# Optimization experiments

Hardware: AMD Instinct MI355X
Metric: run time of the kernel (lower is better)

Reference implementation:

```python
import jax, jax.numpy as jnp
import numpy as np

EPS = 1e-9
THRESHOLD = 0.5


def _spatial_entropy(feat, w1, b1, w2, b2):
    # feat: [B, C, H, W]
    p = jax.nn.sigmoid(feat)
    # faithful to source: log(p+eps) - (1-p)*log(1-p+eps)
    ent = jnp.log(p + EPS) - (1.0 - p) * jnp.log(1.0 - p + EPS)  # [B,C,H,W]
    pooled = feat.mean(axis=(2, 3))                               # [B,C]
    h = jax.nn.relu(pooled @ w1 + b1)                             # [B,64]
    cw = jax.nn.sigmoid(h @ w2 + b2)                              # [B,C]
    se = jnp.einsum('bchw,bc->bhw', ent, cw)                      # [B,H,W]
    # F.normalize(x, dim=(1,2)): L2-normalize jointly over H,W
    norm = jnp.sqrt(jnp.sum(se * se, axis=(1, 2), keepdims=True))
    return se / jnp.maximum(norm, 1e-12)


def _low_entropy_mask(entropy_map):
    # entropy_map: [B,H,W] -> mask [B,1,H,W]
    thr = entropy_map.mean(axis=(1, 2), keepdims=True) * THRESHOLD
    return (entropy_map < thr).astype(entropy_map.dtype)[:, None, :, :]


def setup_inputs() -> dict:
    key = jax.random.key(0)
    k1, k2, k3, k4 = jax.random.split(key, 4)
    B, C, H, W = 16, 256, 64, 64
    vis_feat = jax.random.normal(k1, (B, C, H, W), dtype=jnp.float32)
    text_feat = jax.random.normal(k2, (B, C, H, W), dtype=jnp.float32)
    # channel attention MLP params (Linear(256,64) -> Linear(64,256))
    w1 = jax.random.normal(k3, (256, 64), dtype=jnp.float32) * 0.0625
    b1 = jnp.zeros((64,), dtype=jnp.float32)
    w2 = jax.random.normal(k4, (64, 256), dtype=jnp.float32) * 0.125
    b2 = jnp.zeros((256,), dtype=jnp.float32)
    return {"vis_feat": vis_feat, "text_feat": text_feat,
            "w1": w1, "b1": b1, "w2": w2, "b2": b2}


def reference(vis_feat, text_feat, w1, b1, w2, b2):
    vis_entropy = _spatial_entropy(vis_feat, w1, b1, w2, b2)    # [B,H,W]
    text_entropy = _spatial_entropy(text_feat, w1, b1, w2, b2)  # [B,H,W]
    vis_low = _low_entropy_mask(vis_entropy)                     # [B,1,H,W]
    text_low = _low_entropy_mask(text_entropy)                   # [B,1,H,W]
    enhanced = vis_feat * vis_low + text_feat * text_low * (1.0 - vis_low)
    return enhanced, vis_entropy, text_entropy
```

## Files before the change

kernel.cpp:

```cpp
#include <hip/hip_runtime.h>
#include <math.h>

#define B 16
#define C 256
#define HW 4096
#define EPSE 1e-9f
#define NTHREADS 256
#define CCHUNK 32

__device__ __forceinline__ float fast_rcp(float x) { return __builtin_amdgcn_rcpf(x); }

__device__ __forceinline__ float entf(float x) {
    float e  = __expf(-x);
    float p  = fast_rcp(1.f + e);
    float l1 = __logf(p + EPSE);
    float q  = 1.f - p;
    float l2 = __logf(q + EPSE);
    return fmaf(-q, l2, l1);
}

__global__ void k_pooled(const float* __restrict__ vis,
                         const float* __restrict__ txt,
                         float* __restrict__ pooled,
                         float* __restrict__ se) {
    int blk = blockIdx.x;
    if (blk < 128) {
        float4 z = make_float4(0.f, 0.f, 0.f, 0.f);
        ((float4*)se)[blk * NTHREADS + threadIdx.x] = z;
    }
    int f   = blk >> 12;
    int bc  = blk & (B * C - 1);
    const float* src = (f == 0 ? vis : txt) + (size_t)bc * HW;
    const float4* s4 = (const float4*)src;

    float s = 0.f;
    #pragma unroll
    for (int i = threadIdx.x; i < HW / 4; i += NTHREADS) {
        float4 v = s4[i];
        s += v.x + v.y + v.z + v.w;
    }
    for (int off = 32; off > 0; off >>= 1) s += __shfl_down(s, off);
    __shared__ float sm[4];
    if ((threadIdx.x & 63) == 0) sm[threadIdx.x >> 6] = s;
    __syncthreads();
    if (threadIdx.x == 0) {
        float tot = sm[0] + sm[1] + sm[2] + sm[3];
        pooled[blk] = tot * (1.0f / HW);
    }
}

__global__ void k_mlp(const float* __restrict__ pooled,
                      const float* __restrict__ w1, const float* __restrict__ b1,
                      const float* __restrict__ w2, const float* __restrict__ b2,
                      float* __restrict__ cw) {
    __shared__ float pl[B * C];
    __shared__ float h[B * 64];
    int f = blockIdx.x;
    const float* P = pooled + f * B * C;
    for (int i = threadIdx.x; i < B * C; i += NTHREADS) pl[i] = P[i];
    __syncthreads();
    for (int o = threadIdx.x; o < B * 64; o += NTHREADS) {
        int b = o >> 6, j = o & 63;
        float acc = b1[j];
        for (int c = 0; c < C; ++c) acc = fmaf(pl[b * C + c], w1[c * 64 + j], acc);
        h[o] = fmaxf(acc, 0.f);
    }
    __syncthreads();
    for (int o = threadIdx.x; o < B * C; o += NTHREADS) {
        int b = o >> 8, c2 = o & 255;
        float acc = b2[c2];
        for (int j = 0; j < 64; ++j) acc = fmaf(h[b * 64 + j], w2[j * 256 + c2], acc);
        cw[f * B * C + o] = fast_rcp(1.f + __expf(-acc));
    }
}

__global__ void k_se(const float* __restrict__ vis,
                     const float* __restrict__ txt,
                     const float* __restrict__ cw,
                     float* __restrict__ se) {
    int bx   = blockIdx.x;
    int cc   = bx & 7;
    int tile = (bx >> 3) & 3;
    int b    = (bx >> 5) & 15;
    int f    = bx >> 9;
    const float* src = (f == 0 ? vis : txt)
                       + (size_t)b * C * HW + (size_t)cc * CCHUNK * HW
                       + tile * 1024 + threadIdx.x * 4;

    __shared__ float cwl[CCHUNK];
    if (threadIdx.x < CCHUNK)
        cwl[threadIdx.x] = cw[f * B * C + b * C + cc * CCHUNK + threadIdx.x];
    __syncthreads();

    float4 acc = make_float4(0.f, 0.f, 0.f, 0.f);
    #pragma unroll 4
    for (int c = 0; c < CCHUNK; ++c) {
        float4 x = *(const float4*)(src + (size_t)c * HW);
        float w = cwl[c];
        acc.x = fmaf(entf(x.x), w, acc.x);
        acc.y = fmaf(entf(x.y), w, acc.y);
        acc.z = fmaf(entf(x.z), w, acc.z);
        acc.w = fmaf(entf(x.w), w, acc.w);
    }
    float* dst = se + (f * B + b) * HW + tile * 1024 + threadIdx.x * 4;
    atomicAdd(dst + 0, acc.x);
    atomicAdd(dst + 1, acc.y);
    atomicAdd(dst + 2, acc.z);
    atomicAdd(dst + 3, acc.w);
}

__global__ void k_stats(const float* __restrict__ se,
                        float* __restrict__ inv_norm,
                        float* __restrict__ thr) {
    int fb = blockIdx.x;
    const float4* s4 = (const float4*)(se + fb * HW);
    float s = 0.f, ss = 0.f;
    #pragma unroll
    for (int i = threadIdx.x; i < HW / 4; i += NTHREADS) {
        float4 v = s4[i];
        s  += v.x + v.y + v.z + v.w;
        ss = fmaf(v.x, v.x, ss); ss = fmaf(v.y, v.y, ss);
        ss = fmaf(v.z, v.z, ss); ss = fmaf(v.w, v.w, ss);
    }
    for (int off = 32; off > 0; off >>= 1) {
        s  += __shfl_down(s, off);
        ss += __shfl_down(ss, off);
    }
    __shared__ float sm[8];
    if ((threadIdx.x & 63) == 0) {
        sm[(threadIdx.x >> 6) * 2]     = s;
        sm[(threadIdx.x >> 6) * 2 + 1] = ss;
    }
    __syncthreads();
    if (threadIdx.x == 0) {
        float st  = sm[0] + sm[2] + sm[4] + sm[6];
        float sst = sm[1] + sm[3] + sm[5] + sm[7];
        inv_norm[fb] = 1.f / fmaxf(sqrtf(sst), 1e-12f);
        thr[fb]      = 0.5f * (st * (1.0f / HW));
    }
}

__global__ void k_selwrite(const float* __restrict__ se,
                           const float* __restrict__ inv_norm,
                           const float* __restrict__ thr,
                           float* __restrict__ out_ent_vis,
                           float* __restrict__ out_ent_text,
                           unsigned char* __restrict__ sel) {
    int id = blockIdx.x * NTHREADS + threadIdx.x;
    int b  = id >> 12;
    float sv = se[id];
    float st = se[B * HW + id];
    out_ent_vis[id]  = sv * inv_norm[b];
    out_ent_text[id] = st * inv_norm[B + b];
    bool vl = sv < thr[b];
    bool tl = st < thr[B + b];
    sel[id] = vl ? (unsigned char)1 : (tl ? (unsigned char)2 : (unsigned char)0);
}

__global__ void k_final(const float* __restrict__ vis,
                        const float* __restrict__ txt,
                        const unsigned char* __restrict__ sel,
                        float* __restrict__ out) {
    const int total4 = B * C * HW / 4;
    int stride = gridDim.x * blockDim.x;
    for (int i = blockIdx.x * blockDim.x + threadIdx.x; i < total4; i += stride) {
        float4 v = ((const float4*)vis)[i];
        float4 t = ((const float4*)txt)[i];
        int idx = i << 2;
        int b   = idx >> 20;
        int hw  = idx & (HW - 1);
        uchar4 s = *(const uchar4*)(sel + (b << 12) + hw);
        float4 o;
        o.x = (s.x == 1) ? v.x : ((s.x == 2) ? t.x : 0.f);
        o.y = (s.y == 1) ? v.y : ((s.y == 2) ? t.y : 0.f);
        o.z = (s.z == 1) ? v.z : ((s.z == 2) ? t.z : 0.f);
        o.w = (s.w == 1) ? v.w : ((s.w == 2) ? t.w : 0.f);
        ((float4*)out)[i] = o;
    }
}

extern "C" void kernel_launch(void* const* d_in, const int* in_sizes, int n_in,
                              void* d_out, int out_size, void* d_ws, size_t ws_size,
                              hipStream_t stream) {
    const float* vis = (const float*)d_in[0];
    const float* txt = (const float*)d_in[1];
    const float* w1  = (const float*)d_in[2];
    const float* b1  = (const float*)d_in[3];
    const float* w2  = (const float*)d_in[4];
    const float* b2  = (const float*)d_in[5];

    float* out_enh      = (float*)d_out;
    float* out_ent_vis  = out_enh + (size_t)B * C * HW;
    float* out_ent_text = out_ent_vis + B * HW;

    float* ws       = (float*)d_ws;
    float* pooled   = ws;
    float* cw       = ws + 8192;
    float* se       = ws + 16384;
    float* inv_norm = ws + 147456;
    float* thr      = ws + 147488;
    unsigned char* sel = (unsigned char*)(ws + 147520);

    k_pooled  <<<2 * B * C, NTHREADS, 0, stream>>>(vis, txt, pooled, se);
    k_mlp     <<<2,         NTHREADS, 0, stream>>>(pooled, w1, b1, w2, b2, cw);
    k_se      <<<1024,      NTHREADS, 0, stream>>>(vis, txt, cw, se);
    k_stats   <<<2 * B,     NTHREADS, 0, stream>>>(se, inv_norm, thr);
    k_selwrite<<<B * HW / NTHREADS, NTHREADS, 0, stream>>>(se, inv_norm, thr,
                                                           out_ent_vis, out_ent_text, sel);
    k_final   <<<2048,      NTHREADS, 0, stream>>>(vis, txt, sel, out_enh);
}
```

Before: 267.5 us.

## Fuse selection into final pass, per-wave pooling, smaller channel chunks, nontemporal stores

Removes the separate selection kernel and its byte mask: the final kernel now reads the entropy maps, computes the masks and normalized entropy outputs itself, and applies them over 16-channel groups with nontemporal stores. The pooling kernel assigns one wave per channel plane with four independent accumulators and no shared-memory reduction. The entropy kernel halves the channel chunk, doubling its grid to add parallelism at the cost of twice as many atomics. The intent is fewer launches, less intermediate traffic, and keeping the large output stream from polluting cache.

```diff
diff --git a/kernel.cpp b/kernel.cpp
--- a/kernel.cpp
+++ b/kernel.cpp
@@ -6,7 +6,14 @@
 #define HW 4096
 #define EPSE 1e-9f
 #define NTHREADS 256
-#define CCHUNK 32
+#define CCHUNK 16
+
+typedef float nfloat4 __attribute__((ext_vector_type(4)));
+
+__device__ __forceinline__ void nt_store4(float* p, float4 v) {
+    nfloat4 nv = { v.x, v.y, v.z, v.w };
+    __builtin_nontemporal_store(nv, (nfloat4*)p);
+}
 
 __device__ __forceinline__ float fast_rcp(float x) { return __builtin_amdgcn_rcpf(x); }
 
@@ -25,28 +32,29 @@
                          float* __restrict__ se) {
     int blk = blockIdx.x;
     if (blk < 128) {
-        float4 z = make_float4(0.f, 0.f, 0.f, 0.f);
-        ((float4*)se)[blk * NTHREADS + threadIdx.x] = z;
-    }
-    int f   = blk >> 12;
-    int bc  = blk & (B * C - 1);
-    const float* src = (f == 0 ? vis : txt) + (size_t)bc * HW;
-    const float4* s4 = (const float4*)src;
-
-    float s = 0.f;
+        ((float4*)se)[blk * NTHREADS + threadIdx.x] = make_float4(0.f, 0.f, 0.f, 0.f);
+    }
+    int wave = (blk << 2) | (threadIdx.x >> 6);
+    int lane = threadIdx.x & 63;
+    int f    = wave >> 12;
+    int bc   = wave & (B * C - 1);
+    const float4* src = (const float4*)((f == 0 ? vis : txt) + (size_t)bc * HW);
+
+    float s0 = 0.f, s1 = 0.f, s2 = 0.f, s3 = 0.f;
     #pragma unroll
-    for (int i = threadIdx.x; i < HW / 4; i += NTHREADS) {
-        float4 v = s4[i];
-        s += v.x + v.y + v.z + v.w;
-    }
+    for (int k = 0; k < 16; k += 4) {
+        float4 a = src[lane + (k + 0) * 64];
+        float4 b = src[lane + (k + 1) * 64];
+        float4 c = src[lane + (k + 2) * 64];
+        float4 d = src[lane + (k + 3) * 64];
+        s0 += a.x + a.y + a.z + a.w;
+        s1 += b.x + b.y + b.z + b.w;
+        s2 += c.x + c.y + c.z + c.w;
+        s3 += d.x + d.y + d.z + d.w;
+    }
+    float s = (s0 + s1) + (s2 + s3);
     for (int off = 32; off > 0; off >>= 1) s += __shfl_down(s, off);
-    __shared__ float sm[4];
-    if ((threadIdx.x & 63) == 0) sm[threadIdx.x >> 6] = s;
-    __syncthreads();
-    if (threadIdx.x == 0) {
-        float tot = sm[0] + sm[1] + sm[2] + sm[3];
-        pooled[blk] = tot * (1.0f / HW);
-    }
+    if (lane == 0) pooled[wave] = s * (1.0f / HW);
 }
 
 __global__ void k_mlp(const float* __restrict__ pooled,
@@ -79,10 +87,10 @@
                      const float* __restrict__ cw,
                      float* __restrict__ se) {
     int bx   = blockIdx.x;
-    int cc   = bx & 7;
-    int tile = (bx >> 3) & 3;
-    int b    = (bx >> 5) & 15;
-    int f    = bx >> 9;
+    int cc   = bx & 15;
+    int tile = (bx >> 4) & 3;
+    int b    = (bx >> 6) & 15;
+    int f    = bx >> 10;
     const float* src = (f == 0 ? vis : txt)
                        + (size_t)b * C * HW + (size_t)cc * CCHUNK * HW
                        + tile * 1024 + threadIdx.x * 4;
@@ -140,42 +148,51 @@
     }
 }
 
-__global__ void k_selwrite(const float* __restrict__ se,
-                           const float* __restrict__ inv_norm,
-                           const float* __restrict__ thr,
-                           float* __restrict__ out_ent_vis,
-                           float* __restrict__ out_ent_text,
-                           unsigned char* __restrict__ sel) {
-    int id = blockIdx.x * NTHREADS + threadIdx.x;
-    int b  = id >> 12;
-    float sv = se[id];
-    float st = se[B * HW + id];
-    out_ent_vis[id]  = sv * inv_norm[b];
-    out_ent_text[id] = st * inv_norm[B + b];
-    bool vl = sv < thr[b];
-    bool tl = st < thr[B + b];
-    sel[id] = vl ? (unsigned char)1 : (tl ? (unsigned char)2 : (unsigned char)0);
-}
-
 __global__ void k_final(const float* __restrict__ vis,
                         const float* __restrict__ txt,
-                        const unsigned char* __restrict__ sel,
-                        float* __restrict__ out) {
-    const int total4 = B * C * HW / 4;
-    int stride = gridDim.x * blockDim.x;
-    for (int i = blockIdx.x * blockDim.x + threadIdx.x; i < total4; i += stride) {
-        float4 v = ((const float4*)vis)[i];
-        float4 t = ((const float4*)txt)[i];
-        int idx = i << 2;
-        int b   = idx >> 20;
-        int hw  = idx & (HW - 1);
-        uchar4 s = *(const uchar4*)(sel + (b << 12) + hw);
+                        const float* __restrict__ se,
+                        const float* __restrict__ inv_norm,
+                        const float* __restrict__ thr,
+                        float* __restrict__ out_enh,
+                        float* __restrict__ out_ent_vis,
+                        float* __restrict__ out_ent_text) {
+    int bx   = blockIdx.x;
+    int cg   = bx & 15;
+    int tile = (bx >> 4) & 3;
+    int b    = bx >> 6;
+
+    int hw   = tile * 1024 + threadIdx.x * 4;
+    int mapi = b * HW + hw;
+
+    float4 sv = *(const float4*)(se + mapi);
+    float4 st = *(const float4*)(se + B * HW + mapi);
+    float tv = thr[b], tt = thr[B + b];
+
+    if (cg == 0) {
+        float inv = inv_norm[b], int_ = inv_norm[B + b];
+        float4 ov = make_float4(sv.x * inv, sv.y * inv, sv.z * inv, sv.w * inv);
+        float4 ot = make_float4(st.x * int_, st.y * int_, st.z * int_, st.w * int_);
+        nt_store4(out_ent_vis + mapi, ov);
+        nt_store4(out_ent_text + mapi, ot);
+    }
+
+    int m0 = sv.x < tv ? 1 : (st.x < tt ? 2 : 0);
+    int m1 = sv.y < tv ? 1 : (st.y < tt ? 2 : 0);
+    int m2 = sv.z < tv ? 1 : (st.z < tt ? 2 : 0);
+    int m3 = sv.w < tv ? 1 : (st.w < tt ? 2 : 0);
+
+    size_t base = (size_t)b * C * HW + (size_t)cg * 16 * HW + hw;
+    #pragma unroll 4
+    for (int c = 0; c < 16; ++c) {
+        size_t idx = base + (size_t)c * HW;
+        float4 v = *(const float4*)(vis + idx);
+        float4 t = *(const float4*)(txt + idx);
         float4 o;
-        o.x = (s.x == 1) ? v.x : ((s.x == 2) ? t.x : 0.f);
-        o.y = (s.y == 1) ? v.y : ((s.y == 2) ? t.y : 0.f);
-        o.z = (s.z == 1) ? v.z : ((s.z == 2) ? t.z : 0.f);
-        o.w = (s.w == 1) ? v.w : ((s.w == 2) ? t.w : 0.f);
-        ((float4*)out)[i] = o;
+        o.x = (m0 == 1) ? v.x : ((m0 == 2) ? t.x : 0.f);
+        o.y = (m1 == 1) ? v.y : ((m1 == 2) ? t.y : 0.f);
+        o.z = (m2 == 1) ? v.z : ((m2 == 2) ? t.z : 0.f);
+        o.w = (m3 == 1) ? v.w : ((m3 == 2) ? t.w : 0.f);
+        nt_store4(out_enh + idx, o);
     }
 }
 
@@ -199,13 +216,11 @@
     float* se       = ws + 16384;
     float* inv_norm = ws + 147456;
     float* thr      = ws + 147488;
-    unsigned char* sel = (unsigned char*)(ws + 147520);
-
-    k_pooled  <<<2 * B * C, NTHREADS, 0, stream>>>(vis, txt, pooled, se);
-    k_mlp     <<<2,         NTHREADS, 0, stream>>>(pooled, w1, b1, w2, b2, cw);
-    k_se      <<<1024,      NTHREADS, 0, stream>>>(vis, txt, cw, se);
-    k_stats   <<<2 * B,     NTHREADS, 0, stream>>>(se, inv_norm, thr);
-    k_selwrite<<<B * HW / NTHREADS, NTHREADS, 0, stream>>>(se, inv_norm, thr,
-                                                           out_ent_vis, out_ent_text, sel);
-    k_final   <<<2048,      NTHREADS, 0, stream>>>(vis, txt, sel, out_enh);
-}
+
+    k_pooled<<<2048, NTHREADS, 0, stream>>>(vis, txt, pooled, se);
+    k_mlp   <<<2,    NTHREADS, 0, stream>>>(pooled, w1, b1, w2, b2, cw);
+    k_se    <<<2048, NTHREADS, 0, stream>>>(vis, txt, cw, se);
+    k_stats <<<32,   NTHREADS, 0, stream>>>(se, inv_norm, thr);
+    k_final <<<1024, NTHREADS, 0, stream>>>(vis, txt, se, inv_norm, thr,
+                                            out_enh, out_ent_vis, out_ent_text);
+}
```

Result: no change. 264.0 us (-1.3%).
